# Kernel optimization log

Measured on AMD Instinct MI355X. Metric: run time of the kernel, lower is better.

The kernel has to match this reference:

```python
import jax, jax.numpy as jnp
import numpy as np

N_NODES = 50000
N_EDGES = 800000
D_NODE = 128
D_EDGE = 128
H = 4
HID = 16
D_OUT = 128
EPS = 1e-5


def layer_norm(x, g, b):
    mu = jnp.mean(x, axis=-1, keepdims=True)
    var = jnp.mean(jnp.square(x - mu), axis=-1, keepdims=True)
    return (x - mu) * jax.lax.rsqrt(var + EPS) * g + b


def setup_inputs() -> dict:
    key = jax.random.key(0)
    ks = jax.random.split(key, 8)
    d_hh = H * HID
    return {
        "node_feats": jax.random.normal(ks[0], (N_NODES, D_NODE), dtype=jnp.float32),
        "edge_feats": jax.random.normal(ks[1], (N_EDGES, D_EDGE), dtype=jnp.float32),
        "src": jax.random.randint(ks[2], (N_EDGES,), 0, N_NODES, dtype=jnp.int32),
        "dst": jax.random.randint(ks[3], (N_EDGES,), 0, N_NODES, dtype=jnp.int32),
        # weights stored [in, out] (= torch Linear weight transposed), bias=False everywhere
        "W_node": jax.random.normal(ks[4], (D_NODE, d_hh), dtype=jnp.float32) / np.sqrt(D_NODE),
        "ln_node_g": jnp.ones((d_hh,), jnp.float32),
        "ln_node_b": jnp.zeros((d_hh,), jnp.float32),
        "W_edge": jax.random.normal(ks[5], (D_EDGE, d_hh), dtype=jnp.float32) / np.sqrt(D_EDGE),
        "ln_edge_g": jnp.ones((d_hh,), jnp.float32),
        "ln_edge_b": jnp.zeros((d_hh,), jnp.float32),
        "W_out": jax.random.normal(ks[6], (d_hh, D_OUT), dtype=jnp.float32) / np.sqrt(d_hh),
        "ln_out_g": jnp.ones((D_OUT,), jnp.float32),
        "ln_out_b": jnp.zeros((D_OUT,), jnp.float32),
    }


def reference(node_feats, edge_feats, src, dst,
              W_node, ln_node_g, ln_node_b,
              W_edge, ln_edge_g, ln_edge_b,
              W_out, ln_out_g, ln_out_b):
    n = node_feats.shape[0]
    # project_node: Linear -> GELU (erf, torch default) -> LayerNorm
    hv = layer_norm(jax.nn.gelu(node_feats @ W_node, approximate=False), ln_node_g, ln_node_b)
    hv = hv.reshape(n, H, HID)
    # project_edge: Linear -> LayerNorm, then exp
    he = jnp.exp(layer_norm(edge_feats @ W_edge, ln_edge_g, ln_edge_b))
    he = he.reshape(-1, H, HID)
    # update_all(u_mul_e('hv','he','m'), sum('m','h')): gather-multiply-scatter-sum
    m = hv[src] * he                                   # [E, H, HID]
    h = jax.ops.segment_sum(m, dst, num_segments=n)    # [N, H, HID]
    fn = h.reshape(n, H * HID)
    # project_out: Linear -> GELU -> LayerNorm
    return layer_norm(jax.nn.gelu(fn @ W_out, approximate=False), ln_out_g, ln_out_b)
```

## Files before the change

kernel.cpp:

```cpp
#include <hip/hip_runtime.h>
#include <hip/hip_bf16.h>

#define LN_EPS 1e-5f

typedef __attribute__((ext_vector_type(8))) short short8_t;
typedef __attribute__((ext_vector_type(4))) float float4_t;

__device__ __forceinline__ unsigned short f2bf(float x) {
    unsigned u = __builtin_bit_cast(unsigned, x);
    unsigned r = (u + 0x7FFFu + ((u >> 16) & 1u)) >> 16;
    return (unsigned short)r;
}

__device__ __forceinline__ float bf2f(unsigned short x) {
    return __builtin_bit_cast(float, (unsigned)x << 16);
}

__device__ __forceinline__ float gelu_erf(float p) {
    return 0.5f * p * (1.0f + erff(p * 0.70710678118654752f));
}

__device__ __forceinline__ void atomic_pk_add_bf16_pk(unsigned* addr, unsigned pk) {
    unsigned long long a64 = (unsigned long long)addr;
    asm volatile("global_atomic_pk_add_bf16 %0, %1, off"
                 :: "v"(a64), "v"(pk) : "memory");
}

__device__ __forceinline__ void stage_w64(const float* __restrict__ W,
                                          unsigned short* Wbuf, int t) {
    const int c  = t & 63;
    const int kb = (t >> 6) * 32;
#pragma unroll
    for (int kk = 0; kk < 32; kk += 8) {
        unsigned short tmp[8];
#pragma unroll
        for (int i = 0; i < 8; ++i)
            tmp[i] = f2bf(W[(size_t)(kb + kk + i) * 64 + c]);
        unsigned idx = (unsigned)(c * 128 + kb + kk) ^ (unsigned)((c & 7) << 3);
        *(uint4*)&Wbuf[idx] = *(const uint4*)tmp;
    }
}

__global__ __launch_bounds__(256) void node_proj_kernel(
    const float* __restrict__ X, const float* __restrict__ W,
    const float* __restrict__ g, const float* __restrict__ b,
    unsigned short* __restrict__ outb, int N)
{
    __shared__ __align__(16) unsigned short Wbuf[64 * 128];
    stage_w64(W, Wbuf, threadIdx.x);
    const int lane = threadIdx.x & 63;
    const int r16  = lane & 15;
    const int ks   = (lane >> 4) * 8;
    const int cq   = lane >> 4;
    float gv[4], bv[4];
#pragma unroll
    for (int ct = 0; ct < 4; ++ct) { gv[ct] = g[ct * 16 + r16]; bv[ct] = b[ct * 16 + r16]; }
    __syncthreads();

    const int gw = (int)((blockIdx.x * blockDim.x + threadIdx.x) >> 6);
    const int nw = (int)((gridDim.x * blockDim.x) >> 6);
    const int ntiles = (N + 15) >> 4;
    int tile = gw;
    if (tile >= ntiles) return;

    float4 pf[8];
    {
        const float* base = X + (size_t)min(tile * 16 + r16, N - 1) * 128;
#pragma unroll
        for (int kt = 0; kt < 4; ++kt) {
            pf[2 * kt]     = *(const float4*)(base + kt * 32 + ks);
            pf[2 * kt + 1] = *(const float4*)(base + kt * 32 + ks + 4);
        }
    }

    while (true) {
        const int r0 = tile * 16;
        short8_t a[4];
#pragma unroll
        for (int kt = 0; kt < 4; ++kt) {
            const float4 u = pf[2 * kt], v = pf[2 * kt + 1];
            short8_t t8;
            t8[0] = (short)f2bf(u.x); t8[1] = (short)f2bf(u.y);
            t8[2] = (short)f2bf(u.z); t8[3] = (short)f2bf(u.w);
            t8[4] = (short)f2bf(v.x); t8[5] = (short)f2bf(v.y);
            t8[6] = (short)f2bf(v.z); t8[7] = (short)f2bf(v.w);
            a[kt] = t8;
        }
        const int nt = tile + nw;
        if (nt < ntiles) {
            const float* base = X + (size_t)min(nt * 16 + r16, N - 1) * 128;
#pragma unroll
            for (int kt = 0; kt < 4; ++kt) {
                pf[2 * kt]     = *(const float4*)(base + kt * 32 + ks);
                pf[2 * kt + 1] = *(const float4*)(base + kt * 32 + ks + 4);
            }
        }

        float4_t acc[4];
#pragma unroll
        for (int ct = 0; ct < 4; ++ct) { acc[ct].x = 0.f; acc[ct].y = 0.f; acc[ct].z = 0.f; acc[ct].w = 0.f; }
#pragma unroll
        for (int ct = 0; ct < 4; ++ct) {
            const int c = ct * 16 + r16;
#pragma unroll
            for (int kt = 0; kt < 4; ++kt) {
                unsigned idx = (unsigned)(c * 128 + kt * 32 + ks) ^ (unsigned)((c & 7) << 3);
                short8_t bf = *(const short8_t*)&Wbuf[idx];
                acc[ct] = __builtin_amdgcn_mfma_f32_16x16x32_bf16(a[kt], bf, acc[ct], 0, 0, 0);
            }
        }

#pragma unroll
        for (int j = 0; j < 4; ++j) {
            float p0 = gelu_erf(acc[0][j]), p1 = gelu_erf(acc[1][j]);
            float p2 = gelu_erf(acc[2][j]), p3 = gelu_erf(acc[3][j]);
            float s = (p0 + p1) + (p2 + p3);
            s += __shfl_xor(s, 1); s += __shfl_xor(s, 2);
            s += __shfl_xor(s, 4); s += __shfl_xor(s, 8);
            const float mean = s * (1.0f / 64.0f);
            float d0 = p0 - mean, d1 = p1 - mean, d2 = p2 - mean, d3 = p3 - mean;
            float vs = d0 * d0 + d1 * d1 + d2 * d2 + d3 * d3;
            vs += __shfl_xor(vs, 1); vs += __shfl_xor(vs, 2);
            vs += __shfl_xor(vs, 4); vs += __shfl_xor(vs, 8);
            const float inv = rsqrtf(vs * (1.0f / 64.0f) + LN_EPS);
            const int r = r0 + cq * 4 + j;
            if (r < N) {
                float dd[4] = { d0, d1, d2, d3 };
#pragma unroll
                for (int ct = 0; ct < 4; ++ct)
                    outb[(size_t)r * 64 + ct * 16 + r16] = f2bf(dd[ct] * inv * gv[ct] + bv[ct]);
            }
        }
        if (nt >= ntiles) break;
        tile = nt;
    }
}

__global__ __launch_bounds__(256) void edge_kernel(
    const float* __restrict__ EF, const float* __restrict__ W,
    const float* __restrict__ g, const float* __restrict__ b,
    const int* __restrict__ src, const int* __restrict__ dst,
    const unsigned* __restrict__ hvpk, unsigned* __restrict__ hb, int E)
{
    __shared__ __align__(16) unsigned short Wbuf[64 * 128];
    __shared__ __align__(16) float heL[4][16 * 68];
    __shared__ int srcL[4][16];
    __shared__ int dstL[4][4][16];
    stage_w64(W, Wbuf, threadIdx.x);
    const int lane = threadIdx.x & 63;
    const int r16  = lane & 15;
    const int ks   = (lane >> 4) * 8;
    const int cq   = lane >> 4;
    const int wv   = threadIdx.x >> 6;
    const int cc   = lane & 31;
    const int hf   = lane >> 5;
    float gv[4], bv[4];
#pragma unroll
    for (int ct = 0; ct < 4; ++ct) { gv[ct] = g[ct * 16 + r16]; bv[ct] = b[ct * 16 + r16]; }
    __syncthreads();

    const int gw  = (int)((blockIdx.x * blockDim.x + threadIdx.x) >> 6);
    const int nwv = (int)((gridDim.x * blockDim.x) >> 6);
    const int ntiles = (E + 15) >> 4;
    const int chunk  = (ntiles + nwv - 1) / nwv;
    const int c0 = gw * chunk;
    const int c1 = min(c0 + chunk, ntiles);
    if (c0 >= c1) return;

    float4 pf[8];
    int ps, pd;
    {
        const float* base = EF + (size_t)min(c0 * 16 + r16, E - 1) * 128;
#pragma unroll
        for (int kt = 0; kt < 4; ++kt) {
            pf[2 * kt]     = *(const float4*)(base + kt * 32 + ks);
            pf[2 * kt + 1] = *(const float4*)(base + kt * 32 + ks + 4);
        }
        const int ei = min(c0 * 16 + r16, E - 1);
        ps = src[ei]; pd = dst[ei];
    }

    for (int gbase = c0; gbase < c1; gbase += 4) {
        const int nb = min(4, c1 - gbase);
        unsigned pkP[4][8];

#pragma unroll
        for (int bslot = 0; bslot < 4; ++bslot) {
            if (bslot < nb) {
                const int tile = gbase + bslot;
                const int e0   = tile * 16;

                if (lane < 16) { srcL[wv][lane] = ps; dstL[wv][bslot][lane] = pd; }

                short8_t a[4];
#pragma unroll
                for (int kt = 0; kt < 4; ++kt) {
                    const float4 u = pf[2 * kt], v = pf[2 * kt + 1];
                    short8_t t8;
                    t8[0] = (short)f2bf(u.x); t8[1] = (short)f2bf(u.y);
                    t8[2] = (short)f2bf(u.z); t8[3] = (short)f2bf(u.w);
                    t8[4] = (short)f2bf(v.x); t8[5] = (short)f2bf(v.y);
                    t8[6] = (short)f2bf(v.z); t8[7] = (short)f2bf(v.w);
                    a[kt] = t8;
                }

                const int nt = tile + 1;
                if (nt < c1) {
                    const float* base = EF + (size_t)min(nt * 16 + r16, E - 1) * 128;
#pragma unroll
                    for (int kt = 0; kt < 4; ++kt) {
                        pf[2 * kt]     = *(const float4*)(base + kt * 32 + ks);
                        pf[2 * kt + 1] = *(const float4*)(base + kt * 32 + ks + 4);
                    }
                    const int ei = min(nt * 16 + r16, E - 1);
                    ps = src[ei]; pd = dst[ei];
                }

                float4_t acc[4];
#pragma unroll
                for (int ct = 0; ct < 4; ++ct) { acc[ct].x = 0.f; acc[ct].y = 0.f; acc[ct].z = 0.f; acc[ct].w = 0.f; }
#pragma unroll
                for (int ct = 0; ct < 4; ++ct) {
                    const int c = ct * 16 + r16;
#pragma unroll
                    for (int kt = 0; kt < 4; ++kt) {
                        unsigned idx = (unsigned)(c * 128 + kt * 32 + ks) ^ (unsigned)((c & 7) << 3);
                        short8_t bf = *(const short8_t*)&Wbuf[idx];
                        acc[ct] = __builtin_amdgcn_mfma_f32_16x16x32_bf16(a[kt], bf, acc[ct], 0, 0, 0);
                    }
                }

#pragma unroll
                for (int j = 0; j < 4; ++j) {
                    float s = acc[0][j] + acc[1][j] + acc[2][j] + acc[3][j];
                    s += __shfl_xor(s, 1); s += __shfl_xor(s, 2);
                    s += __shfl_xor(s, 4); s += __shfl_xor(s, 8);
                    const float mean = s * (1.0f / 64.0f);
                    float d0 = acc[0][j] - mean, d1 = acc[1][j] - mean;
                    float d2 = acc[2][j] - mean, d3 = acc[3][j] - mean;
                    float vs = d0 * d0 + d1 * d1 + d2 * d2 + d3 * d3;
                    vs += __shfl_xor(vs, 1); vs += __shfl_xor(vs, 2);
                    vs += __shfl_xor(vs, 4); vs += __shfl_xor(vs, 8);
                    const float inv = rsqrtf(vs * (1.0f / 64.0f) + LN_EPS);
                    const int rloc = cq * 4 + j;
                    float dd[4] = { d0, d1, d2, d3 };
#pragma unroll
                    for (int ct = 0; ct < 4; ++ct)
                        heL[wv][rloc * 68 + ct * 16 + r16] = __expf(dd[ct] * inv * gv[ct] + bv[ct]);
                }

#pragma unroll
                for (int u = 0; u < 8; ++u) {
                    const int er = u * 2 + hf;
                    const int s  = srcL[wv][er];
                    const unsigned hvd = hvpk[(size_t)s * 32 + cc];
                    const float2 he2 = *(const float2*)&heL[wv][er * 68 + 2 * cc];
                    float lo = he2.x * bf2f((unsigned short)(hvd & 0xFFFFu));
                    float hi = he2.y * bf2f((unsigned short)(hvd >> 16));
                    if (e0 + er >= E) { lo = 0.f; hi = 0.f; }
                    pkP[bslot][u] = (unsigned)f2bf(lo) | ((unsigned)f2bf(hi) << 16);
                }
            }
        }

#pragma unroll
        for (int bslot = 0; bslot < 4; ++bslot) {
            if (bslot < nb) {
#pragma unroll
                for (int u = 0; u < 8; ++u) {
                    const int er = u * 2 + hf;
                    const int d  = dstL[wv][bslot][er];
                    atomic_pk_add_bf16_pk(hb + (size_t)d * 32 + cc, pkP[bslot][u]);
                }
            }
        }
    }
}

__global__ __launch_bounds__(256) void out_proj_kernel(
    const unsigned short* __restrict__ Hb, const float* __restrict__ W,
    const float* __restrict__ g, const float* __restrict__ b,
    float* __restrict__ out, int N)
{
    __shared__ __align__(16) unsigned short Wbuf[128 * 64];
    {
        const int t  = threadIdx.x;
        const int c  = t & 127;
        const int k0 = (t >> 7) * 32;
#pragma unroll
        for (int kk = 0; kk < 32; kk += 8) {
            unsigned short tmp[8];
#pragma unroll
            for (int i = 0; i < 8; ++i)
                tmp[i] = f2bf(W[(size_t)(k0 + kk + i) * 128 + c]);
            unsigned idx = (unsigned)(c * 64 + k0 + kk) ^ (unsigned)((c & 7) << 3);
            *(uint4*)&Wbuf[idx] = *(const uint4*)tmp;
        }
    }
    const int lane = threadIdx.x & 63;
    const int r16  = lane & 15;
    const int ks   = (lane >> 4) * 8;
    const int cq   = lane >> 4;
    float gv[8], bv[8];
#pragma unroll
    for (int ct = 0; ct < 8; ++ct) { gv[ct] = g[ct * 16 + r16]; bv[ct] = b[ct * 16 + r16]; }
    __syncthreads();

    const int gw = (int)((blockIdx.x * blockDim.x + threadIdx.x) >> 6);
    const int nw = (int)((gridDim.x * blockDim.x) >> 6);
    const int ntiles = (N + 15) >> 4;
    int tile = gw;
    if (tile >= ntiles) return;

    short8_t pa[2];
    {
        const unsigned short* base = Hb + (size_t)min(tile * 16 + r16, N - 1) * 64;
        pa[0] = *(const short8_t*)(base + ks);
        pa[1] = *(const short8_t*)(base + 32 + ks);
    }

    while (true) {
        const int r0 = tile * 16;
        short8_t a[2];
        a[0] = pa[0]; a[1] = pa[1];

        const int nt = tile + nw;
        if (nt < ntiles) {
            const unsigned short* base = Hb + (size_t)min(nt * 16 + r16, N - 1) * 64;
            pa[0] = *(const short8_t*)(base + ks);
            pa[1] = *(const short8_t*)(base + 32 + ks);
        }

        float4_t acc[8];
#pragma unroll
        for (int ct = 0; ct < 8; ++ct) { acc[ct].x = 0.f; acc[ct].y = 0.f; acc[ct].z = 0.f; acc[ct].w = 0.f; }
#pragma unroll
        for (int ct = 0; ct < 8; ++ct) {
            const int c = ct * 16 + r16;
#pragma unroll
            for (int kt = 0; kt < 2; ++kt) {
                unsigned idx = (unsigned)(c * 64 + kt * 32 + ks) ^ (unsigned)((c & 7) << 3);
                short8_t bf = *(const short8_t*)&Wbuf[idx];
                acc[ct] = __builtin_amdgcn_mfma_f32_16x16x32_bf16(a[kt], bf, acc[ct], 0, 0, 0);
            }
        }

#pragma unroll
        for (int j = 0; j < 4; ++j) {
            float p[8];
            float s = 0.f;
#pragma unroll
            for (int ct = 0; ct < 8; ++ct) { p[ct] = gelu_erf(acc[ct][j]); s += p[ct]; }
            s += __shfl_xor(s, 1); s += __shfl_xor(s, 2);
            s += __shfl_xor(s, 4); s += __shfl_xor(s, 8);
            const float mean = s * (1.0f / 128.0f);
            float vs = 0.f;
#pragma unroll
            for (int ct = 0; ct < 8; ++ct) { p[ct] -= mean; vs += p[ct] * p[ct]; }
            vs += __shfl_xor(vs, 1); vs += __shfl_xor(vs, 2);
            vs += __shfl_xor(vs, 4); vs += __shfl_xor(vs, 8);
            const float inv = rsqrtf(vs * (1.0f / 128.0f) + LN_EPS);
            const int r = r0 + cq * 4 + j;
            if (r < N) {
#pragma unroll
                for (int ct = 0; ct < 8; ++ct)
                    out[(size_t)r * 128 + ct * 16 + r16] = p[ct] * inv * gv[ct] + bv[ct];
            }
        }
        if (nt >= ntiles) break;
        tile = nt;
    }
}

extern "C" void kernel_launch(void* const* d_in, const int* in_sizes, int n_in,
                              void* d_out, int out_size, void* d_ws, size_t ws_size,
                              hipStream_t stream) {
    const float* node_feats = (const float*)d_in[0];
    const float* edge_feats = (const float*)d_in[1];
    const int*   src        = (const int*)d_in[2];
    const int*   dst        = (const int*)d_in[3];
    const float* W_node     = (const float*)d_in[4];
    const float* ln_ng      = (const float*)d_in[5];
    const float* ln_nb      = (const float*)d_in[6];
    const float* W_edge     = (const float*)d_in[7];
    const float* ln_eg      = (const float*)d_in[8];
    const float* ln_eb      = (const float*)d_in[9];
    const float* W_out      = (const float*)d_in[10];
    const float* ln_og      = (const float*)d_in[11];
    const float* ln_ob      = (const float*)d_in[12];
    float* out = (float*)d_out;

    const int N = in_sizes[0] / 128;
    const int E = in_sizes[2];

    unsigned short* hvb = (unsigned short*)d_ws;
    unsigned short* hb  = hvb + (size_t)N * 64;

    hipMemsetAsync(hb, 0, (size_t)N * 64 * sizeof(unsigned short), stream);
    node_proj_kernel<<<784, 256, 0, stream>>>(node_feats, W_node, ln_ng, ln_nb, hvb, N);
    edge_kernel<<<1024, 256, 0, stream>>>(edge_feats, W_edge, ln_eg, ln_eb,
                                          src, dst, (const unsigned*)hvb, (unsigned*)hb, E);
    out_proj_kernel<<<784, 256, 0, stream>>>(hb, W_out, ln_og, ln_ob, out, N);
}
```

Before: 171.6 us.

## Sort edges by destination and coalesce per-lane scatter atomics

Adds histogram, scan and scatter kernels that build a destination-sorted edge permutation each call. The edge kernel reads edges through this permutation and accumulates contributions for consecutive equal destinations in registers, issuing one packed bf16 atomic per run instead of one per edge. This is meant to reduce atomic traffic and contention on the node accumulator. In exchange it adds four kernel launches and makes the edge feature reads indirect gathers rather than sequential streams.

After: 263.1 us. 1.53x slower.

```diff
diff --git a/kernel.cpp b/kernel.cpp
--- a/kernel.cpp
+++ b/kernel.cpp
@@ -20,7 +20,8 @@
     return 0.5f * p * (1.0f + erff(p * 0.70710678118654752f));
 }
 
-__device__ __forceinline__ void atomic_pk_add_bf16_pk(unsigned* addr, unsigned pk) {
+__device__ __forceinline__ void atomic_pk_add_bf16_f(unsigned* addr, float lo, float hi) {
+    const unsigned pk = (unsigned)f2bf(lo) | ((unsigned)f2bf(hi) << 16);
     unsigned long long a64 = (unsigned long long)addr;
     asm volatile("global_atomic_pk_add_bf16 %0, %1, off"
                  :: "v"(a64), "v"(pk) : "memory");
@@ -38,6 +39,70 @@
             tmp[i] = f2bf(W[(size_t)(kb + kk + i) * 64 + c]);
         unsigned idx = (unsigned)(c * 128 + kb + kk) ^ (unsigned)((c & 7) << 3);
         *(uint4*)&Wbuf[idx] = *(const uint4*)tmp;
+    }
+}
+
+__global__ __launch_bounds__(256) void hist_kernel(
+    const int* __restrict__ dst, int* __restrict__ cnt, int E)
+{
+    const int i = blockIdx.x * blockDim.x + threadIdx.x;
+    const int n = gridDim.x * blockDim.x;
+    for (int e = i; e < E; e += n) atomicAdd(&cnt[dst[e]], 1);
+}
+
+__global__ __launch_bounds__(256) void scanA_kernel(
+    const int* __restrict__ cnt, int* __restrict__ off,
+    int* __restrict__ bsum, int n)
+{
+    __shared__ int ls[256];
+    const int t = threadIdx.x;
+    const int base = blockIdx.x * 1024 + t * 4;
+    int v[4];
+    int s = 0;
+#pragma unroll
+    for (int i = 0; i < 4; ++i) {
+        v[i] = (base + i < n) ? cnt[base + i] : 0;
+        s += v[i];
+    }
+    ls[t] = s;
+    __syncthreads();
+    for (int d = 1; d < 256; d <<= 1) {
+        int x = (t >= d) ? ls[t - d] : 0;
+        __syncthreads();
+        ls[t] += x;
+        __syncthreads();
+    }
+    int p = ls[t] - s;
+#pragma unroll
+    for (int i = 0; i < 4; ++i) {
+        if (base + i < n) off[base + i] = p;
+        p += v[i];
+    }
+    if (t == 255) bsum[blockIdx.x] = ls[255];
+}
+
+__global__ __launch_bounds__(64) void scanB_kernel(int* __restrict__ bsum, int nb)
+{
+    const int t = threadIdx.x;
+    const int o = (t < nb) ? bsum[t] : 0;
+    int v = o;
+    for (int d = 1; d < 64; d <<= 1) {
+        int x = __shfl_up(v, d);
+        if (t >= d) v += x;
+    }
+    if (t < nb) bsum[t] = v - o;
+}
+
+__global__ __launch_bounds__(256) void scatter_kernel(
+    const int* __restrict__ dst, int* __restrict__ off,
+    const int* __restrict__ bsum, int* __restrict__ perm, int E)
+{
+    const int i = blockIdx.x * blockDim.x + threadIdx.x;
+    const int n = gridDim.x * blockDim.x;
+    for (int e = i; e < E; e += n) {
+        const int d = dst[e];
+        const int p = atomicAdd(&off[d], 1) + bsum[d >> 10];
+        perm[p] = e;
     }
 }
 
@@ -140,6 +205,7 @@
     const float* __restrict__ EF, const float* __restrict__ W,
     const float* __restrict__ g, const float* __restrict__ b,
     const int* __restrict__ src, const int* __restrict__ dst,
+    const int* __restrict__ perm,
     const unsigned* __restrict__ hvpk, unsigned* __restrict__ hb, int E)
 {
     __shared__ __align__(16) unsigned short Wbuf[64 * 128];
@@ -170,15 +236,18 @@
     float4 pf[8];
     int ps, pd;
     {
-        const float* base = EF + (size_t)min(c0 * 16 + r16, E - 1) * 128;
+        const int pm = perm[min(c0 * 16 + r16, E - 1)];
+        const float* base = EF + (size_t)pm * 128;
 #pragma unroll
         for (int kt = 0; kt < 4; ++kt) {
             pf[2 * kt]     = *(const float4*)(base + kt * 32 + ks);
             pf[2 * kt + 1] = *(const float4*)(base + kt * 32 + ks + 4);
         }
-        const int ei = min(c0 * 16 + r16, E - 1);
-        ps = src[ei]; pd = dst[ei];
-    }
+        ps = src[pm]; pd = dst[pm];
+    }
+
+    int   curD = -1;
+    float aLo = 0.f, aHi = 0.f;
 
     for (int gbase = c0; gbase < c1; gbase += 4) {
         const int nb = min(4, c1 - gbase);
@@ -206,14 +275,14 @@
 
                 const int nt = tile + 1;
                 if (nt < c1) {
-                    const float* base = EF + (size_t)min(nt * 16 + r16, E - 1) * 128;
+                    const int pm = perm[min(nt * 16 + r16, E - 1)];
+                    const float* base = EF + (size_t)pm * 128;
 #pragma unroll
                     for (int kt = 0; kt < 4; ++kt) {
                         pf[2 * kt]     = *(const float4*)(base + kt * 32 + ks);
                         pf[2 * kt + 1] = *(const float4*)(base + kt * 32 + ks + 4);
                     }
-                    const int ei = min(nt * 16 + r16, E - 1);
-                    ps = src[ei]; pd = dst[ei];
+                    ps = src[pm]; pd = dst[pm];
                 }
 
                 float4_t acc[4];
@@ -270,11 +339,21 @@
                 for (int u = 0; u < 8; ++u) {
                     const int er = u * 2 + hf;
                     const int d  = dstL[wv][bslot][er];
-                    atomic_pk_add_bf16_pk(hb + (size_t)d * 32 + cc, pkP[bslot][u]);
-                }
-            }
-        }
-    }
+                    const unsigned pk = pkP[bslot][u];
+                    const float lo = bf2f((unsigned short)(pk & 0xFFFFu));
+                    const float hi = bf2f((unsigned short)(pk >> 16));
+                    if (d != curD) {
+                        if (curD >= 0)
+                            atomic_pk_add_bf16_f(hb + (size_t)curD * 32 + cc, aLo, aHi);
+                        curD = d; aLo = lo; aHi = hi;
+                    } else { aLo += lo; aHi += hi; }
+                }
+            }
+        }
+    }
+
+    if (curD >= 0)
+        atomic_pk_add_bf16_f(hb + (size_t)curD * 32 + cc, aLo, aHi);
 }
 
 __global__ __launch_bounds__(256) void out_proj_kernel(
@@ -393,12 +472,24 @@
     const int N = in_sizes[0] / 128;
     const int E = in_sizes[2];
 
-    unsigned short* hvb = (unsigned short*)d_ws;
-    unsigned short* hb  = hvb + (size_t)N * 64;
+    unsigned short* hvb  = (unsigned short*)d_ws;
+    unsigned short* hb   = hvb + (size_t)N * 64;
+    int*            cnt  = (int*)(hb + (size_t)N * 64);
+    int*            off  = cnt + N;
+    int*            bsum = off + N;
+    int*            perm = bsum + 64;
+
+    const int nbA = (N + 1023) >> 10;
 
     hipMemsetAsync(hb, 0, (size_t)N * 64 * sizeof(unsigned short), stream);
+    hipMemsetAsync(cnt, 0, (size_t)N * sizeof(int), stream);
+    hist_kernel<<<1024, 256, 0, stream>>>(dst, cnt, E);
+    scanA_kernel<<<nbA, 256, 0, stream>>>(cnt, off, bsum, N);
+    scanB_kernel<<<1, 64, 0, stream>>>(bsum, nbA);
+    scatter_kernel<<<1024, 256, 0, stream>>>(dst, off, bsum, perm, E);
     node_proj_kernel<<<784, 256, 0, stream>>>(node_feats, W_node, ln_ng, ln_nb, hvb, N);
     edge_kernel<<<1024, 256, 0, stream>>>(edge_feats, W_edge, ln_eg, ln_eb,
-                                          src, dst, (const unsigned*)hvb, (unsigned*)hb, E);
+                                          src, dst, perm,
+                                          (const unsigned*)hvb, (unsigned*)hb, E);
     out_proj_kernel<<<784, 256, 0, stream>>>(hb, W_out, ln_og, ln_ob, out, N);
 }
```
